# Kernel optimization log

Measured on AMD Instinct MI355X. Metric: run time of the kernel, lower is better.

The kernel has to match this reference:

```python
import jax, jax.numpy as jnp
import numpy as np

N, E = 100000, 800000
H, C = 4, 32
HC = H * C


def setup_inputs() -> dict:
    key = jax.random.key(0)
    ks = jax.random.split(key, 32)

    def lin(k, fi, fo):
        return jax.random.normal(k, (fi, fo), jnp.float32) / np.sqrt(fi)

    inp = {
        "x": jax.random.normal(ks[0], (N, 2), jnp.float32),
        "edge_index": jax.random.randint(ks[1], (2, E), 0, N, jnp.int64),
        "edge_attr": jax.random.normal(ks[2], (E, 1), jnp.float32),
        # layer 0 (in=2)
        "Wq0": lin(ks[3], 2, HC), "bq0": jnp.zeros((HC,), jnp.float32),
        "Wk0": lin(ks[4], 2, HC), "bk0": jnp.zeros((HC,), jnp.float32),
        "Wv0": lin(ks[5], 2, HC), "bv0": jnp.zeros((HC,), jnp.float32),
        "We0": lin(ks[6], 1, HC),
        "Ws0": lin(ks[7], 2, HC), "bs0": jnp.zeros((HC,), jnp.float32),
        # layer 1 (in=HC)
        "Wq1": lin(ks[8], HC, HC), "bq1": jnp.zeros((HC,), jnp.float32),
        "Wk1": lin(ks[9], HC, HC), "bk1": jnp.zeros((HC,), jnp.float32),
        "Wv1": lin(ks[10], HC, HC), "bv1": jnp.zeros((HC,), jnp.float32),
        "We1": lin(ks[11], 1, HC),
        "Ws1": lin(ks[12], HC, HC), "bs1": jnp.zeros((HC,), jnp.float32),
        # classifier
        "Wc1": lin(ks[13], HC, 128), "bc1": jnp.zeros((128,), jnp.float32),
        "Wc2": lin(ks[14], 128, 64), "bc2": jnp.zeros((64,), jnp.float32),
        "Wc3": lin(ks[15], 64, 1), "bc3": jnp.zeros((1,), jnp.float32),
    }
    return inp


def _tconv(x, src, dst, edge_attr, Wq, bq, Wk, bk, Wv, bv, We, Ws, bs):
    # PyG TransformerConv (concat=True, root_weight=True, beta=False)
    n = x.shape[0]
    q = (x @ Wq + bq).reshape(n, H, C)
    k = (x @ Wk + bk).reshape(n, H, C)
    v = (x @ Wv + bv).reshape(n, H, C)
    e = (edge_attr @ We).reshape(-1, H, C)            # [E,H,C]
    k_j = k[src] + e
    v_j = v[src] + e
    alpha = jnp.einsum("ehc,ehc->eh", q[dst], k_j) / np.sqrt(C)  # [E,H]
    m = jax.ops.segment_max(alpha, dst, num_segments=n)          # [n,H]
    m = jnp.where(jnp.isfinite(m), m, 0.0)            # nodes with no in-edges
    ex = jnp.exp(alpha - m[dst])
    denom = jax.ops.segment_sum(ex, dst, num_segments=n)
    w = ex / (denom[dst] + 1e-16)                      # per-edge softmax weight
    out = jax.ops.segment_sum(v_j * w[:, :, None], dst, num_segments=n)
    return out.reshape(n, HC) + x @ Ws + bs


def reference(x, edge_index, edge_attr,
              Wq0, bq0, Wk0, bk0, Wv0, bv0, We0, Ws0, bs0,
              Wq1, bq1, Wk1, bk1, Wv1, bv1, We1, Ws1, bs1,
              Wc1, bc1, Wc2, bc2, Wc3, bc3):
    src, dst = edge_index[0], edge_index[1]
    h = jax.nn.relu(_tconv(x, src, dst, edge_attr, Wq0, bq0, Wk0, bk0, Wv0, bv0, We0, Ws0, bs0))
    h = jax.nn.relu(_tconv(h, src, dst, edge_attr, Wq1, bq1, Wk1, bk1, Wv1, bv1, We1, Ws1, bs1))
    # classifier (dropout inactive in eval)
    h = jax.nn.relu(h @ Wc1 + bc1)
    h = jax.nn.relu(h @ Wc2 + bc2)
    return h @ Wc3 + bc3
```

## Files before the change

kernel.cpp:

```cpp
#include <hip/hip_runtime.h>
#include <hip/hip_bf16.h>
#include <cstdio>
#include <cstdint>


typedef short s16x8 __attribute__((ext_vector_type(8)));
typedef float f32x4 __attribute__((ext_vector_type(4)));

static inline int cdiv(int a, int b) { return (a + b - 1) / b; }

__device__ __forceinline__ float bflo(unsigned u) {
    union { unsigned i; float f; } x; x.i = u << 16; return x.f;
}
__device__ __forceinline__ float bfhi(unsigned u) {
    union { unsigned i; float f; } x; x.i = u & 0xffff0000u; return x.f;
}
__device__ __forceinline__ unsigned short f2b(float f) {
    __hip_bfloat16 h = __float2bfloat16(f);
    return *reinterpret_cast<unsigned short*>(&h);
}
__device__ __forceinline__ unsigned packbf(float lo, float hi) {
    return (unsigned)f2b(lo) | ((unsigned)f2b(hi) << 16);
}


__global__ __launch_bounds__(256) void hist_kernel(const int* __restrict__ dst, int E,
                                                   int* __restrict__ counts) {
    int e = blockIdx.x * 256 + threadIdx.x;
    if (e < E) atomicAdd(&counts[dst[e]], 1);
}

__global__ __launch_bounds__(256) void scan_sums(const int* __restrict__ counts, int n,
                                                 int* __restrict__ bsums) {
    __shared__ int red[256];
    int base = blockIdx.x * 2048 + threadIdx.x * 8;
    int s = 0;
#pragma unroll
    for (int j = 0; j < 8; ++j) {
        int i = base + j;
        if (i < n) s += counts[i];
    }
    red[threadIdx.x] = s;
    __syncthreads();
    for (int off = 128; off > 0; off >>= 1) {
        if (threadIdx.x < off) red[threadIdx.x] += red[threadIdx.x + off];
        __syncthreads();
    }
    if (threadIdx.x == 0) bsums[blockIdx.x] = red[0];
}

__global__ void scan_mid(int* bsums, int nb, int* offsets, int n) {
    if (blockIdx.x == 0 && threadIdx.x == 0) {
        int run = 0;
        for (int i = 0; i < nb; ++i) { int t = bsums[i]; bsums[i] = run; run += t; }
        offsets[n] = run;
    }
}

__global__ __launch_bounds__(256) void scan_out(const int* __restrict__ counts, int n,
                                                const int* __restrict__ bsums,
                                                int* __restrict__ offsets) {
    __shared__ int tsum[256];
    int base = blockIdx.x * 2048 + threadIdx.x * 8;
    int v[8];
    int s = 0;
#pragma unroll
    for (int j = 0; j < 8; ++j) {
        int i = base + j;
        v[j] = (i < n) ? counts[i] : 0;
        s += v[j];
    }
    tsum[threadIdx.x] = s;
    __syncthreads();
    for (int off = 1; off < 256; off <<= 1) {
        int x = (threadIdx.x >= (unsigned)off) ? tsum[threadIdx.x - off] : 0;
        __syncthreads();
        tsum[threadIdx.x] += x;
        __syncthreads();
    }
    int excl = tsum[threadIdx.x] - s + bsums[blockIdx.x];
#pragma unroll
    for (int j = 0; j < 8; ++j) {
        int i = base + j;
        if (i < n) { offsets[i] = excl; excl += v[j]; }
    }
}

__global__ __launch_bounds__(256) void scatter_kernel(const int* __restrict__ src,
                                                      const int* __restrict__ dst,
                                                      const float* __restrict__ ea, int E,
                                                      const int* __restrict__ offsets,
                                                      int* __restrict__ fill,
                                                      int* __restrict__ csr_src,
                                                      float* __restrict__ csr_ea) {
    int e = blockIdx.x * 256 + threadIdx.x;
    if (e >= E) return;
    int d = dst[e];
    int p = offsets[d] + atomicAdd(&fill[d], 1);
    csr_src[p] = src[e];
    csr_ea[p] = ea[e];
}


__global__ __launch_bounds__(256) void pack_w_kernel(
    const float* __restrict__ Wq1, const float* __restrict__ Wk1,
    const float* __restrict__ Wv1, const float* __restrict__ Ws1,
    const float* __restrict__ Wc1, const float* __restrict__ Wc2,
    unsigned short* __restrict__ wpk) {
    int idx = blockIdx.x * 256 + threadIdx.x;
    if (idx >= 90112) return;
    int local, COLS;
    const float* W;
    if (idx < 81920) {
        int m = idx >> 14;
        local = idx & 16383;
        COLS = 128;
        W = (m == 0) ? Wq1 : (m == 1) ? Wk1 : (m == 2) ? Wv1 : (m == 3) ? Ws1 : Wc1;
    } else {
        local = idx - 81920;
        COLS = 64;
        W = Wc2;
    }
    int CT = COLS >> 4;
    int j = local & 7, lane = (local >> 3) & 63, t = local >> 9;
    int ct = t % CT, kc = t / CT;
    int k = kc * 32 + ((lane >> 4) << 3) + j;
    int nn = (ct << 4) + (lane & 15);
    wpk[idx] = f2b(W[k * COLS + nn]);
}


__global__ void prep0_kernel(const float* __restrict__ Wq, const float* __restrict__ bq,
                             const float* __restrict__ Wk, const float* __restrict__ bk,
                             const float* __restrict__ We, float* __restrict__ gcoef) {
    int t = threadIdx.x;
    if (t >= 48) return;
    int h = t / 12, r = t % 12, i = r >> 2, j = r & 3;
    const float* A = (i == 0) ? Wq : (i == 1) ? (Wq + 128) : bq;
    const float* B = (j == 0) ? Wk : (j == 1) ? (Wk + 128) : (j == 2) ? We : bk;
    float s = 0.f;
    for (int c = 0; c < 32; ++c) s += A[h * 32 + c] * B[h * 32 + c];
    gcoef[h * 12 + i * 4 + j] = s * 0.17677669529663687f;
}


__global__ __launch_bounds__(256) void agg0_kernel(
    const float* __restrict__ x, const float* __restrict__ gcoef,
    float4* __restrict__ agg4,
    const int* __restrict__ offsets, const int* __restrict__ csr_src,
    const float* __restrict__ csr_ea, int n_nodes) {
    int tid = blockIdx.x * 256 + threadIdx.x;
    int n = tid >> 2, h = tid & 3;
    if (n >= n_nodes) return;
    float2 xn = ((const float2*)x)[n];
    const float4* G4 = (const float4*)gcoef;
    float4 g0 = G4[h * 3 + 0], g1 = G4[h * 3 + 1], g2 = G4[h * 3 + 2];
    float c0 = fmaf(xn.y, g1.x, fmaf(xn.x, g0.x, g2.x));
    float c1 = fmaf(xn.y, g1.y, fmaf(xn.x, g0.y, g2.y));
    float c2 = fmaf(xn.y, g1.z, fmaf(xn.x, g0.z, g2.z));
    float c3 = fmaf(xn.y, g1.w, fmaf(xn.x, g0.w, g2.w));
    int beg = offsets[n], end = offsets[n + 1];
    float m = -1e30f, d = 0.f, X0 = 0.f, X1 = 0.f, EA = 0.f;
    for (int j = beg; j < end; ++j) {
        int s = csr_src[j];
        float e = csr_ea[j];
        float2 xs = ((const float2*)x)[s];
        float al = fmaf(c0, xs.x, fmaf(c1, xs.y, fmaf(c2, e, c3)));
        float nm = fmaxf(m, al);
        float cc = __expf(m - nm), w = __expf(al - nm);
        d = fmaf(d, cc, w);
        X0 = fmaf(X0, cc, w * xs.x);
        X1 = fmaf(X1, cc, w * xs.y);
        EA = fmaf(EA, cc, w * e);
        m = nm;
    }
    agg4[(size_t)n * 4 + h] = make_float4(X0, X1, EA, d);
}


__global__ __launch_bounds__(256) void expand0_kernel(
    const float* __restrict__ x, const float4* __restrict__ agg4,
    const float* __restrict__ Wv, const float* __restrict__ bv,
    const float* __restrict__ We, const float* __restrict__ Ws,
    const float* __restrict__ bs, uint2* __restrict__ H0, int n_nodes) {
    int gid = blockIdx.x * 256 + threadIdx.x;
    int n = gid >> 5, g = gid & 31;
    if (n >= n_nodes) return;
    int h = g >> 3;
    float4 ag = agg4[(size_t)n * 4 + h];
    float inv = 1.f / (ag.w + 1e-16f);
    float2 xn = ((const float2*)x)[n];
    float4 wv0 = ((const float4*)Wv)[g], wv1 = ((const float4*)(Wv + 128))[g];
    float4 we = ((const float4*)We)[g], bv4 = ((const float4*)bv)[g];
    float4 ws0 = ((const float4*)Ws)[g], ws1 = ((const float4*)(Ws + 128))[g];
    float4 bs4 = ((const float4*)bs)[g];
    float o0 = fmaf(wv0.x, ag.x, fmaf(wv1.x, ag.y, fmaf(we.x, ag.z, bv4.x * ag.w))) * inv
             + fmaf(xn.x, ws0.x, fmaf(xn.y, ws1.x, bs4.x));
    float o1 = fmaf(wv0.y, ag.x, fmaf(wv1.y, ag.y, fmaf(we.y, ag.z, bv4.y * ag.w))) * inv
             + fmaf(xn.x, ws0.y, fmaf(xn.y, ws1.y, bs4.y));
    float o2 = fmaf(wv0.z, ag.x, fmaf(wv1.z, ag.y, fmaf(we.z, ag.z, bv4.z * ag.w))) * inv
             + fmaf(xn.x, ws0.z, fmaf(xn.y, ws1.z, bs4.z));
    float o3 = fmaf(wv0.w, ag.x, fmaf(wv1.w, ag.y, fmaf(we.w, ag.z, bv4.w * ag.w))) * inv
             + fmaf(xn.x, ws0.w, fmaf(xn.y, ws1.w, bs4.w));
    uint2 o;
    o.x = packbf(fmaxf(o0, 0.f), fmaxf(o1, 0.f));
    o.y = packbf(fmaxf(o2, 0.f), fmaxf(o3, 0.f));
    H0[(size_t)n * 32 + g] = o;
}


__global__ __launch_bounds__(256) void agg1_kernel(
    const uint2* __restrict__ Q2, const uint2* __restrict__ K2,
    const uint2* __restrict__ V2, const float* __restrict__ We,
    const uint2* __restrict__ S2, uint2* __restrict__ Hout,
    const int* __restrict__ offsets, const int* __restrict__ csr_src,
    const float* __restrict__ csr_ea, int n_nodes) {
    int wid = threadIdx.x >> 6, lane = threadIdx.x & 63;
    int h = lane & 31, half = lane >> 5;
    int n = blockIdx.x * 4 + wid;
    if (n >= n_nodes) return;
    size_t rb = (size_t)n * 32;
    const float rsc = 0.17677669529663687f;
    uint2 qp = Q2[rb + h];
    float q0 = bflo(qp.x) * rsc, q1 = bfhi(qp.x) * rsc;
    float q2 = bflo(qp.y) * rsc, q3 = bfhi(qp.y) * rsc;
    float4 we4 = ((const float4*)We)[h];
    float qwe = fmaf(q3, we4.w, fmaf(q2, we4.z, fmaf(q1, we4.y, q0 * we4.x)));
    qwe += __shfl_xor(qwe, 1);
    qwe += __shfl_xor(qwe, 2);
    qwe += __shfl_xor(qwe, 4);
    int beg = __builtin_amdgcn_readfirstlane(offsets[n]);
    int end = __builtin_amdgcn_readfirstlane(offsets[n + 1]);
    float mA = -1e30f, dA = 0.f, x0A = 0.f, x1A = 0.f, x2A = 0.f, x3A = 0.f, eAs = 0.f;
    float mB = -1e30f, dB = 0.f, x0B = 0.f, x1B = 0.f, x2B = 0.f, x3B = 0.f, eBs = 0.f;
    int nq = (end - beg + 3) >> 2;
    for (int it = 0; it < nq; ++it) {
        int jA = beg + 4 * it + half;
        int jB = jA + 2;
        bool vA = jA < end, vB = jB < end;
        int jmA = vA ? jA : beg, jmB = vB ? jB : beg;
        int sA = csr_src[jmA], sB = csr_src[jmB];
        float eaA = csr_ea[jmA], eaB = csr_ea[jmB];
        uint2 kA = K2[(size_t)sA * 32 + h], vA2 = V2[(size_t)sA * 32 + h];
        uint2 kB = K2[(size_t)sB * 32 + h], vB2 = V2[(size_t)sB * 32 + h];
        {
            float p = fmaf(q3, bfhi(kA.y), fmaf(q2, bflo(kA.y),
                      fmaf(q1, bfhi(kA.x), q0 * bflo(kA.x))));
            p += __shfl_xor(p, 1);
            p += __shfl_xor(p, 2);
            p += __shfl_xor(p, 4);
            float al = fmaf(eaA, qwe, p);
            al = vA ? al : -3.0e38f;
            float nm = fmaxf(mA, al);
            float cc = __expf(mA - nm), w = __expf(al - nm);
            dA = fmaf(dA, cc, w);
            x0A = fmaf(x0A, cc, w * bflo(vA2.x));
            x1A = fmaf(x1A, cc, w * bfhi(vA2.x));
            x2A = fmaf(x2A, cc, w * bflo(vA2.y));
            x3A = fmaf(x3A, cc, w * bfhi(vA2.y));
            eAs = fmaf(eAs, cc, w * eaA);
            mA = nm;
        }
        {
            float p = fmaf(q3, bfhi(kB.y), fmaf(q2, bflo(kB.y),
                      fmaf(q1, bfhi(kB.x), q0 * bflo(kB.x))));
            p += __shfl_xor(p, 1);
            p += __shfl_xor(p, 2);
            p += __shfl_xor(p, 4);
            float al = fmaf(eaB, qwe, p);
            al = vB ? al : -3.0e38f;
            float nm = fmaxf(mB, al);
            float cc = __expf(mB - nm), w = __expf(al - nm);
            dB = fmaf(dB, cc, w);
            x0B = fmaf(x0B, cc, w * bflo(vB2.x));
            x1B = fmaf(x1B, cc, w * bfhi(vB2.x));
            x2B = fmaf(x2B, cc, w * bflo(vB2.y));
            x3B = fmaf(x3B, cc, w * bfhi(vB2.y));
            eBs = fmaf(eBs, cc, w * eaB);
            mB = nm;
        }
    }
    float M = fmaxf(mA, mB);
    float cA = __expf(mA - M), cB = __expf(mB - M);
    float d = fmaf(dA, cA, dB * cB);
    float a0 = fmaf(x0A, cA, x0B * cB);
    float a1 = fmaf(x1A, cA, x1B * cB);
    float a2 = fmaf(x2A, cA, x2B * cB);
    float a3 = fmaf(x3A, cA, x3B * cB);
    float ea = fmaf(eAs, cA, eBs * cB);
    float mo = __shfl_xor(M, 32);
    float dd = __shfl_xor(d, 32);
    float b0 = __shfl_xor(a0, 32), b1 = __shfl_xor(a1, 32);
    float b2 = __shfl_xor(a2, 32), b3 = __shfl_xor(a3, 32);
    float eo = __shfl_xor(ea, 32);
    float MM = fmaxf(M, mo);
    float c0 = __expf(M - MM), c1 = __expf(mo - MM);
    d = d * c0 + dd * c1;
    a0 = a0 * c0 + b0 * c1; a1 = a1 * c0 + b1 * c1;
    a2 = a2 * c0 + b2 * c1; a3 = a3 * c0 + b3 * c1;
    ea = ea * c0 + eo * c1;
    float inv = 1.f / (d + 1e-16f);
    uint2 sp = S2[rb + h];
    if (half == 0) {
        uint2 o;
        o.x = packbf(fmaxf(fmaf((a0 + we4.x * ea), inv, bflo(sp.x)), 0.f),
                     fmaxf(fmaf((a1 + we4.y * ea), inv, bfhi(sp.x)), 0.f));
        o.y = packbf(fmaxf(fmaf((a2 + we4.z * ea), inv, bflo(sp.y)), 0.f),
                     fmaxf(fmaf((a3 + we4.w * ea), inv, bfhi(sp.y)), 0.f));
        Hout[rb + h] = o;
    }
}


__global__ __launch_bounds__(256) void gemm4_kernel(
    const unsigned short* __restrict__ Hb, int n_nodes,
    const unsigned short* __restrict__ wpk,
    const float* __restrict__ B0, unsigned short* __restrict__ O0,
    const float* __restrict__ B1, unsigned short* __restrict__ O1,
    const float* __restrict__ B2, unsigned short* __restrict__ O2,
    const float* __restrict__ B3, unsigned short* __restrict__ O3) {
    int wid = threadIdx.x >> 6, lane = threadIdx.x & 63;
    int lr = lane & 15, lk = lane >> 4;
    int rbase = blockIdx.x * 128 + wid * 32;
    s16x8 b[2][4];
#pragma unroll
    for (int nt = 0; nt < 2; ++nt) {
        int row = min(rbase + nt * 16 + lr, n_nodes - 1);
        const s16x8* hp = (const s16x8*)(Hb + (size_t)row * 128);
#pragma unroll
        for (int kc = 0; kc < 4; ++kc) b[nt][kc] = hp[kc * 4 + lk];
    }
    const float* Bm[4] = {B0, B1, B2, B3};
    unsigned short* Om[4] = {O0, O1, O2, O3};
#pragma unroll
    for (int mm = 0; mm < 4; ++mm) {
        const s16x8* wp = (const s16x8*)(wpk + mm * 16384);
        f32x4 acc[2][8];
#pragma unroll
        for (int nt = 0; nt < 2; ++nt)
#pragma unroll
            for (int ct = 0; ct < 8; ++ct) acc[nt][ct] = (f32x4){0.f, 0.f, 0.f, 0.f};
#pragma unroll
        for (int kc = 0; kc < 4; ++kc) {
#pragma unroll
            for (int ct = 0; ct < 8; ++ct) {
                s16x8 a = wp[(kc * 8 + ct) * 64 + lane];
                acc[0][ct] = __builtin_amdgcn_mfma_f32_16x16x32_bf16(a, b[0][kc], acc[0][ct], 0, 0, 0);
                acc[1][ct] = __builtin_amdgcn_mfma_f32_16x16x32_bf16(a, b[1][kc], acc[1][ct], 0, 0, 0);
            }
        }
        const float* Bp = Bm[mm];
        unsigned short* Op = Om[mm];
#pragma unroll
        for (int ct = 0; ct < 8; ++ct) {
            float4 bb = *(const float4*)(Bp + ct * 16 + lk * 4);
#pragma unroll
            for (int nt = 0; nt < 2; ++nt) {
                int node = rbase + nt * 16 + lr;
                if (node < n_nodes) {
                    uint2 o;
                    o.x = packbf(acc[nt][ct][0] + bb.x, acc[nt][ct][1] + bb.y);
                    o.y = packbf(acc[nt][ct][2] + bb.z, acc[nt][ct][3] + bb.w);
                    ((uint2*)(Op + (size_t)node * 128))[ct * 4 + lk] = o;
                }
            }
        }
    }
}


__global__ __launch_bounds__(256) void classifier_kernel(
    const unsigned short* __restrict__ H1b, int n_nodes,
    const unsigned short* __restrict__ wc1p, const float* __restrict__ bc1,
    const unsigned short* __restrict__ wc2p, const float* __restrict__ bc2,
    const float* __restrict__ Wc3, const float* __restrict__ bc3,
    float* __restrict__ out) {
    __shared__ char lds_raw[4 * 16 * 272];
    int wid = threadIdx.x >> 6, lane = threadIdx.x & 63;
    int lr = lane & 15, lk = lane >> 4;
    int nb = blockIdx.x * 64 + wid * 16;
    char* tile = lds_raw + wid * 16 * 272;

    s16x8 b[4];
    {
        int row = min(nb + lr, n_nodes - 1);
        const s16x8* hp = (const s16x8*)(H1b + (size_t)row * 128);
#pragma unroll
        for (int kc = 0; kc < 4; ++kc) b[kc] = hp[kc * 4 + lk];
    }
    f32x4 acc[8];
#pragma unroll
    for (int ct = 0; ct < 8; ++ct) acc[ct] = (f32x4){0.f, 0.f, 0.f, 0.f};
#pragma unroll
    for (int kc = 0; kc < 4; ++kc)
#pragma unroll
        for (int ct = 0; ct < 8; ++ct) {
            s16x8 a = ((const s16x8*)wc1p)[(kc * 8 + ct) * 64 + lane];
            acc[ct] = __builtin_amdgcn_mfma_f32_16x16x32_bf16(a, b[kc], acc[ct], 0, 0, 0);
        }
#pragma unroll
    for (int ct = 0; ct < 8; ++ct) {
        float4 bb = *(const float4*)(bc1 + ct * 16 + lk * 4);
        uint2 o;
        o.x = packbf(fmaxf(acc[ct][0] + bb.x, 0.f), fmaxf(acc[ct][1] + bb.y, 0.f));
        o.y = packbf(fmaxf(acc[ct][2] + bb.z, 0.f), fmaxf(acc[ct][3] + bb.w, 0.f));
        *(uint2*)(tile + lr * 272 + ct * 32 + lk * 8) = o;
    }
    __syncthreads();
    s16x8 b2[4];
#pragma unroll
    for (int kc = 0; kc < 4; ++kc)
        b2[kc] = *(const s16x8*)(tile + lr * 272 + kc * 64 + lk * 16);
    f32x4 acc2[4];
#pragma unroll
    for (int ct = 0; ct < 4; ++ct) acc2[ct] = (f32x4){0.f, 0.f, 0.f, 0.f};
#pragma unroll
    for (int kc = 0; kc < 4; ++kc)
#pragma unroll
        for (int ct = 0; ct < 4; ++ct) {
            s16x8 a = ((const s16x8*)wc2p)[(kc * 4 + ct) * 64 + lane];
            acc2[ct] = __builtin_amdgcn_mfma_f32_16x16x32_bf16(a, b2[kc], acc2[ct], 0, 0, 0);
        }
    float part = 0.f;
#pragma unroll
    for (int ct = 0; ct < 4; ++ct) {
        int ch0 = ct * 16 + lk * 4;
        float4 bb = *(const float4*)(bc2 + ch0);
        float4 w3 = *(const float4*)(Wc3 + ch0);
        part += fmaxf(acc2[ct][0] + bb.x, 0.f) * w3.x;
        part += fmaxf(acc2[ct][1] + bb.y, 0.f) * w3.y;
        part += fmaxf(acc2[ct][2] + bb.z, 0.f) * w3.z;
        part += fmaxf(acc2[ct][3] + bb.w, 0.f) * w3.w;
    }
    part += __shfl_xor(part, 16);
    part += __shfl_xor(part, 32);
    if (lk == 0) {
        int node = nb + lr;
        if (node < n_nodes) out[node] = part + bc3[0];
    }
}


extern "C" void kernel_launch(void* const* d_in, const int* in_sizes, int n_in,
                              void* d_out, int out_size, void* d_ws, size_t ws_size,
                              hipStream_t stream) {
    const float* x = (const float*)d_in[0];
    const int* ei = (const int*)d_in[1];
    const float* ea = (const float*)d_in[2];
    const float *Wq0 = (const float*)d_in[3], *bq0 = (const float*)d_in[4];
    const float *Wk0 = (const float*)d_in[5], *bk0 = (const float*)d_in[6];
    const float *Wv0 = (const float*)d_in[7], *bv0 = (const float*)d_in[8];
    const float* We0 = (const float*)d_in[9];
    const float *Ws0 = (const float*)d_in[10], *bs0 = (const float*)d_in[11];
    const float *Wq1 = (const float*)d_in[12], *bq1 = (const float*)d_in[13];
    const float *Wk1 = (const float*)d_in[14], *bk1 = (const float*)d_in[15];
    const float *Wv1 = (const float*)d_in[16], *bv1 = (const float*)d_in[17];
    const float* We1 = (const float*)d_in[18];
    const float *Ws1 = (const float*)d_in[19], *bs1 = (const float*)d_in[20];
    const float *Wc1 = (const float*)d_in[21], *bc1 = (const float*)d_in[22];
    const float *Wc2 = (const float*)d_in[23], *bc2 = (const float*)d_in[24];
    const float *Wc3 = (const float*)d_in[25], *bc3 = (const float*)d_in[26];

    const int N = in_sizes[0] / 2;
    const int E = in_sizes[2];
    const int* src = ei;
    const int* dst = ei + E;

    size_t NM = (size_t)N * 128;
    float4* agg4 = (float4*)d_ws;
    float* gcoef = (float*)(agg4 + (size_t)N * 4);
    unsigned short* H0b = (unsigned short*)(gcoef + 64);
    unsigned short* Qb = H0b + NM;
    unsigned short* Kb = Qb + NM;
    unsigned short* Vb = Kb + NM;
    unsigned short* S1b = Vb + NM;
    unsigned short* wpk = S1b + NM;
    int* counts = (int*)(wpk + 90112);
    int* fill = counts + N;
    int* offsets = fill + N;
    int* bsums = offsets + N + 1;
    int* csr_src = bsums + 256;
    float* csr_ea = (float*)(csr_src + E);
    size_t need = (size_t)((char*)(csr_ea + E) - (char*)d_ws);
    if (need > ws_size) {
        fprintf(stderr, "kernel_launch: ws too small (need %zu, have %zu)\n", need, ws_size);
        return;
    }

    const int NB_SCAN = cdiv(N, 2048);

    hipMemsetAsync(counts, 0, (size_t)N * 8, stream);
    hist_kernel<<<cdiv(E, 256), 256, 0, stream>>>(dst, E, counts);
    scan_sums<<<NB_SCAN, 256, 0, stream>>>(counts, N, bsums);
    scan_mid<<<1, 64, 0, stream>>>(bsums, NB_SCAN, offsets, N);
    scan_out<<<NB_SCAN, 256, 0, stream>>>(counts, N, bsums, offsets);
    scatter_kernel<<<cdiv(E, 256), 256, 0, stream>>>(src, dst, ea, E, offsets, fill,
                                                     csr_src, csr_ea);
    pack_w_kernel<<<cdiv(90112, 256), 256, 0, stream>>>(Wq1, Wk1, Wv1, Ws1, Wc1, Wc2, wpk);
    prep0_kernel<<<1, 64, 0, stream>>>(Wq0, bq0, Wk0, bk0, We0, gcoef);

    agg0_kernel<<<cdiv(N * 4, 256), 256, 0, stream>>>(
        x, gcoef, agg4, offsets, csr_src, csr_ea, N);
    expand0_kernel<<<cdiv(N * 32, 256), 256, 0, stream>>>(
        x, agg4, Wv0, bv0, We0, Ws0, bs0, (uint2*)H0b, N);

    gemm4_kernel<<<cdiv(N, 128), 256, 0, stream>>>(
        H0b, N, wpk, bq1, Qb, bk1, Kb, bv1, Vb, bs1, S1b);
    agg1_kernel<<<cdiv(N, 4), 256, 0, stream>>>(
        (const uint2*)Qb, (const uint2*)Kb, (const uint2*)Vb, We1,
        (const uint2*)S1b, (uint2*)S1b, offsets, csr_src, csr_ea, N);

    classifier_kernel<<<cdiv(N, 64), 256, 0, stream>>>(
        S1b, N, wpk + 65536, bc1, wpk + 81920, bc2, Wc3, bc3, (float*)d_out);
}
```

Before: 402.7 us.

## Drop online softmax max tracking, interleave K/V rows, fuse prep and scatter fill

Replaces the running-max online softmax in both aggregation kernels with plain exp2 accumulation, clamping logits to 72 and folding log2(e) into the scale. This removes the rescale exps and extra FMAs per edge. K and V are interleaved into one 256-wide row so each edge gathers both from one neighbourhood, and CSR stores precomputed byte offsets (src<<9). The scatter kernel reuses the counts array via atomicSub, which drops the fill buffer and halves the memset. prep0 is merged into pack_w as an extra block, and agg1 runs as one 64-thread block per node. Skipping the max subtraction risks overflow or precision loss if logits are large, which the clamp only partly guards against.

Result: faster. 385.3 us (-4.3%).

```diff
diff --git a/kernel.cpp b/kernel.cpp
--- a/kernel.cpp
+++ b/kernel.cpp
@@ -8,6 +8,10 @@
 typedef float f32x4 __attribute__((ext_vector_type(4)));
 
 static inline int cdiv(int a, int b) { return (a + b - 1) / b; }
+
+#define EXP2F(x) __builtin_amdgcn_exp2f(x)
+#define LOG2E 1.4426950408889634f
+#define RSC 0.17677669529663687f
 
 __device__ __forceinline__ float bflo(unsigned u) {
     union { unsigned i; float f; } x; x.i = u << 16; return x.f;
@@ -90,14 +94,15 @@
                                                       const int* __restrict__ dst,
                                                       const float* __restrict__ ea, int E,
                                                       const int* __restrict__ offsets,
-                                                      int* __restrict__ fill,
-                                                      int* __restrict__ csr_src,
+                                                      int* __restrict__ counts,
+                                                      int* __restrict__ csr_off,
                                                       float* __restrict__ csr_ea) {
     int e = blockIdx.x * 256 + threadIdx.x;
     if (e >= E) return;
     int d = dst[e];
-    int p = offsets[d] + atomicAdd(&fill[d], 1);
-    csr_src[p] = src[e];
+    int r = atomicSub(&counts[d], 1);
+    int p = offsets[d] + r - 1;
+    csr_off[p] = src[e] << 9;
     csr_ea[p] = ea[e];
 }
 
@@ -106,9 +111,23 @@
     const float* __restrict__ Wq1, const float* __restrict__ Wk1,
     const float* __restrict__ Wv1, const float* __restrict__ Ws1,
     const float* __restrict__ Wc1, const float* __restrict__ Wc2,
-    unsigned short* __restrict__ wpk) {
+    unsigned short* __restrict__ wpk,
+    const float* __restrict__ Wq0, const float* __restrict__ bq0,
+    const float* __restrict__ Wk0, const float* __restrict__ bk0,
+    const float* __restrict__ We0, float* __restrict__ gcoef) {
+    if (blockIdx.x == 352) {
+        int t = threadIdx.x;
+        if (t < 48) {
+            int h = t / 12, r = t % 12, i = r >> 2, j = r & 3;
+            const float* A = (i == 0) ? Wq0 : (i == 1) ? (Wq0 + 128) : bq0;
+            const float* B = (j == 0) ? Wk0 : (j == 1) ? (Wk0 + 128) : (j == 2) ? We0 : bk0;
+            float s = 0.f;
+            for (int c = 0; c < 32; ++c) s += A[h * 32 + c] * B[h * 32 + c];
+            gcoef[h * 12 + i * 4 + j] = s * (RSC * LOG2E);
+        }
+        return;
+    }
     int idx = blockIdx.x * 256 + threadIdx.x;
-    if (idx >= 90112) return;
     int local, COLS;
     const float* W;
     if (idx < 81920) {
@@ -130,24 +149,10 @@
 }
 
 
-__global__ void prep0_kernel(const float* __restrict__ Wq, const float* __restrict__ bq,
-                             const float* __restrict__ Wk, const float* __restrict__ bk,
-                             const float* __restrict__ We, float* __restrict__ gcoef) {
-    int t = threadIdx.x;
-    if (t >= 48) return;
-    int h = t / 12, r = t % 12, i = r >> 2, j = r & 3;
-    const float* A = (i == 0) ? Wq : (i == 1) ? (Wq + 128) : bq;
-    const float* B = (j == 0) ? Wk : (j == 1) ? (Wk + 128) : (j == 2) ? We : bk;
-    float s = 0.f;
-    for (int c = 0; c < 32; ++c) s += A[h * 32 + c] * B[h * 32 + c];
-    gcoef[h * 12 + i * 4 + j] = s * 0.17677669529663687f;
-}
-
-
 __global__ __launch_bounds__(256) void agg0_kernel(
     const float* __restrict__ x, const float* __restrict__ gcoef,
     float4* __restrict__ agg4,
-    const int* __restrict__ offsets, const int* __restrict__ csr_src,
+    const int* __restrict__ offsets, const int* __restrict__ csr_off,
     const float* __restrict__ csr_ea, int n_nodes) {
     int tid = blockIdx.x * 256 + threadIdx.x;
     int n = tid >> 2, h = tid & 3;
@@ -160,19 +165,17 @@
     float c2 = fmaf(xn.y, g1.z, fmaf(xn.x, g0.z, g2.z));
     float c3 = fmaf(xn.y, g1.w, fmaf(xn.x, g0.w, g2.w));
     int beg = offsets[n], end = offsets[n + 1];
-    float m = -1e30f, d = 0.f, X0 = 0.f, X1 = 0.f, EA = 0.f;
+    float d = 0.f, X0 = 0.f, X1 = 0.f, EA = 0.f;
     for (int j = beg; j < end; ++j) {
-        int s = csr_src[j];
+        int off = csr_off[j];
         float e = csr_ea[j];
-        float2 xs = ((const float2*)x)[s];
+        float2 xs = *(const float2*)((const char*)x + (off >> 6));
         float al = fmaf(c0, xs.x, fmaf(c1, xs.y, fmaf(c2, e, c3)));
-        float nm = fmaxf(m, al);
-        float cc = __expf(m - nm), w = __expf(al - nm);
-        d = fmaf(d, cc, w);
-        X0 = fmaf(X0, cc, w * xs.x);
-        X1 = fmaf(X1, cc, w * xs.y);
-        EA = fmaf(EA, cc, w * e);
-        m = nm;
+        float w = EXP2F(fminf(al, 72.f));
+        d += w;
+        X0 = fmaf(w, xs.x, X0);
+        X1 = fmaf(w, xs.y, X1);
+        EA = fmaf(w, e, EA);
     }
     agg4[(size_t)n * 4 + h] = make_float4(X0, X1, EA, d);
 }
@@ -209,21 +212,21 @@
 }
 
 
-__global__ __launch_bounds__(256) void agg1_kernel(
-    const uint2* __restrict__ Q2, const uint2* __restrict__ K2,
-    const uint2* __restrict__ V2, const float* __restrict__ We,
-    const uint2* __restrict__ S2, uint2* __restrict__ Hout,
-    const int* __restrict__ offsets, const int* __restrict__ csr_src,
-    const float* __restrict__ csr_ea, int n_nodes) {
-    int wid = threadIdx.x >> 6, lane = threadIdx.x & 63;
+__global__ __launch_bounds__(64) void agg1_kernel(
+    const uint2* __restrict__ Q2, const unsigned short* __restrict__ KV,
+    const float* __restrict__ We, const uint2* __restrict__ S2,
+    uint2* __restrict__ Hout, const int* __restrict__ offsets,
+    const int* __restrict__ csr_off, const float* __restrict__ csr_ea,
+    int n_nodes) {
+    int lane = threadIdx.x & 63;
     int h = lane & 31, half = lane >> 5;
-    int n = blockIdx.x * 4 + wid;
+    int n = blockIdx.x;
     if (n >= n_nodes) return;
     size_t rb = (size_t)n * 32;
-    const float rsc = 0.17677669529663687f;
+    const float sc = RSC * LOG2E;
     uint2 qp = Q2[rb + h];
-    float q0 = bflo(qp.x) * rsc, q1 = bfhi(qp.x) * rsc;
-    float q2 = bflo(qp.y) * rsc, q3 = bfhi(qp.y) * rsc;
+    float q0 = bflo(qp.x) * sc, q1 = bfhi(qp.x) * sc;
+    float q2 = bflo(qp.y) * sc, q3 = bfhi(qp.y) * sc;
     float4 we4 = ((const float4*)We)[h];
     float qwe = fmaf(q3, we4.w, fmaf(q2, we4.z, fmaf(q1, we4.y, q0 * we4.x)));
     qwe += __shfl_xor(qwe, 1);
@@ -231,35 +234,35 @@
     qwe += __shfl_xor(qwe, 4);
     int beg = __builtin_amdgcn_readfirstlane(offsets[n]);
     int end = __builtin_amdgcn_readfirstlane(offsets[n + 1]);
-    float mA = -1e30f, dA = 0.f, x0A = 0.f, x1A = 0.f, x2A = 0.f, x3A = 0.f, eAs = 0.f;
-    float mB = -1e30f, dB = 0.f, x0B = 0.f, x1B = 0.f, x2B = 0.f, x3B = 0.f, eBs = 0.f;
-    int nq = (end - beg + 3) >> 2;
-    for (int it = 0; it < nq; ++it) {
-        int jA = beg + 4 * it + half;
-        int jB = jA + 2;
-        bool vA = jA < end, vB = jB < end;
-        int jmA = vA ? jA : beg, jmB = vB ? jB : beg;
-        int sA = csr_src[jmA], sB = csr_src[jmB];
-        float eaA = csr_ea[jmA], eaB = csr_ea[jmB];
-        uint2 kA = K2[(size_t)sA * 32 + h], vA2 = V2[(size_t)sA * 32 + h];
-        uint2 kB = K2[(size_t)sB * 32 + h], vB2 = V2[(size_t)sB * 32 + h];
+    float dA = 0.f, a0A = 0.f, a1A = 0.f, a2A = 0.f, a3A = 0.f, eA = 0.f;
+    float dB = 0.f, a0B = 0.f, a1B = 0.f, a2B = 0.f, a3B = 0.f, eB = 0.f;
+    int lane_b = h << 3;
+    for (int j = beg + half; j < end; j += 4) {
+        int jB = j + 2;
+        bool vB = jB < end;
+        int jmB = vB ? jB : j;
+        int offA = csr_off[j], offB = csr_off[jmB];
+        float eaA = csr_ea[j], eaB = csr_ea[jmB];
+        const char* kvA = (const char*)KV + (size_t)(unsigned)offA + lane_b;
+        const char* kvB = (const char*)KV + (size_t)(unsigned)offB + lane_b;
+        uint2 kA = *(const uint2*)kvA;
+        uint2 vA = *(const uint2*)(kvA + 256);
+        uint2 kB = *(const uint2*)kvB;
+        uint2 vB2 = *(const uint2*)(kvB + 256);
         {
             float p = fmaf(q3, bfhi(kA.y), fmaf(q2, bflo(kA.y),
                       fmaf(q1, bfhi(kA.x), q0 * bflo(kA.x))));
             p += __shfl_xor(p, 1);
             p += __shfl_xor(p, 2);
             p += __shfl_xor(p, 4);
-            float al = fmaf(eaA, qwe, p);
-            al = vA ? al : -3.0e38f;
-            float nm = fmaxf(mA, al);
-            float cc = __expf(mA - nm), w = __expf(al - nm);
-            dA = fmaf(dA, cc, w);
-            x0A = fmaf(x0A, cc, w * bflo(vA2.x));
-            x1A = fmaf(x1A, cc, w * bfhi(vA2.x));
-            x2A = fmaf(x2A, cc, w * bflo(vA2.y));
-            x3A = fmaf(x3A, cc, w * bfhi(vA2.y));
-            eAs = fmaf(eAs, cc, w * eaA);
-            mA = nm;
+            float al = fminf(fmaf(eaA, qwe, p), 72.f);
+            float w = EXP2F(al);
+            dA += w;
+            a0A = fmaf(w, bflo(vA.x), a0A);
+            a1A = fmaf(w, bfhi(vA.x), a1A);
+            a2A = fmaf(w, bflo(vA.y), a2A);
+            a3A = fmaf(w, bfhi(vA.y), a3A);
+            eA = fmaf(w, eaA, eA);
         }
         {
             float p = fmaf(q3, bfhi(kB.y), fmaf(q2, bflo(kB.y),
@@ -269,44 +272,32 @@
             p += __shfl_xor(p, 4);
             float al = fmaf(eaB, qwe, p);
             al = vB ? al : -3.0e38f;
-            float nm = fmaxf(mB, al);
-            float cc = __expf(mB - nm), w = __expf(al - nm);
-            dB = fmaf(dB, cc, w);
-            x0B = fmaf(x0B, cc, w * bflo(vB2.x));
-            x1B = fmaf(x1B, cc, w * bfhi(vB2.x));
-            x2B = fmaf(x2B, cc, w * bflo(vB2.y));
-            x3B = fmaf(x3B, cc, w * bfhi(vB2.y));
-            eBs = fmaf(eBs, cc, w * eaB);
-            mB = nm;
-        }
-    }
-    float M = fmaxf(mA, mB);
-    float cA = __expf(mA - M), cB = __expf(mB - M);
-    float d = fmaf(dA, cA, dB * cB);
-    float a0 = fmaf(x0A, cA, x0B * cB);
-    float a1 = fmaf(x1A, cA, x1B * cB);
-    float a2 = fmaf(x2A, cA, x2B * cB);
-    float a3 = fmaf(x3A, cA, x3B * cB);
-    float ea = fmaf(eAs, cA, eBs * cB);
-    float mo = __shfl_xor(M, 32);
-    float dd = __shfl_xor(d, 32);
-    float b0 = __shfl_xor(a0, 32), b1 = __shfl_xor(a1, 32);
-    float b2 = __shfl_xor(a2, 32), b3 = __shfl_xor(a3, 32);
-    float eo = __shfl_xor(ea, 32);
-    float MM = fmaxf(M, mo);
-    float c0 = __expf(M - MM), c1 = __expf(mo - MM);
-    d = d * c0 + dd * c1;
-    a0 = a0 * c0 + b0 * c1; a1 = a1 * c0 + b1 * c1;
-    a2 = a2 * c0 + b2 * c1; a3 = a3 * c0 + b3 * c1;
-    ea = ea * c0 + eo * c1;
-    float inv = 1.f / (d + 1e-16f);
-    uint2 sp = S2[rb + h];
+            float w = EXP2F(fminf(al, 72.f));
+            dB += w;
+            a0B = fmaf(w, bflo(vB2.x), a0B);
+            a1B = fmaf(w, bfhi(vB2.x), a1B);
+            a2B = fmaf(w, bflo(vB2.y), a2B);
+            a3B = fmaf(w, bfhi(vB2.y), a3B);
+            eB = fmaf(w, eaB, eB);
+        }
+    }
+    float d = dA + dB;
+    float a0 = a0A + a0B, a1 = a1A + a1B, a2 = a2A + a2B, a3 = a3A + a3B;
+    float ea = eA + eB;
+    d += __shfl_xor(d, 32);
+    a0 += __shfl_xor(a0, 32);
+    a1 += __shfl_xor(a1, 32);
+    a2 += __shfl_xor(a2, 32);
+    a3 += __shfl_xor(a3, 32);
+    ea += __shfl_xor(ea, 32);
     if (half == 0) {
+        float inv = 1.f / (d + 1e-16f);
+        uint2 sp = S2[rb + h];
         uint2 o;
-        o.x = packbf(fmaxf(fmaf((a0 + we4.x * ea), inv, bflo(sp.x)), 0.f),
-                     fmaxf(fmaf((a1 + we4.y * ea), inv, bfhi(sp.x)), 0.f));
-        o.y = packbf(fmaxf(fmaf((a2 + we4.z * ea), inv, bflo(sp.y)), 0.f),
-                     fmaxf(fmaf((a3 + we4.w * ea), inv, bfhi(sp.y)), 0.f));
+        o.x = packbf(fmaxf(fmaf(a0 + we4.x * ea, inv, bflo(sp.x)), 0.f),
+                     fmaxf(fmaf(a1 + we4.y * ea, inv, bfhi(sp.x)), 0.f));
+        o.y = packbf(fmaxf(fmaf(a2 + we4.z * ea, inv, bflo(sp.y)), 0.f),
+                     fmaxf(fmaf(a3 + we4.w * ea, inv, bfhi(sp.y)), 0.f));
         Hout[rb + h] = o;
     }
 }
@@ -315,10 +306,10 @@
 __global__ __launch_bounds__(256) void gemm4_kernel(
     const unsigned short* __restrict__ Hb, int n_nodes,
     const unsigned short* __restrict__ wpk,
-    const float* __restrict__ B0, unsigned short* __restrict__ O0,
-    const float* __restrict__ B1, unsigned short* __restrict__ O1,
-    const float* __restrict__ B2, unsigned short* __restrict__ O2,
-    const float* __restrict__ B3, unsigned short* __restrict__ O3) {
+    const float* __restrict__ B0, unsigned short* __restrict__ O0, int ld0,
+    const float* __restrict__ B1, unsigned short* __restrict__ O1, int ld1,
+    const float* __restrict__ B2, unsigned short* __restrict__ O2, int ld2,
+    const float* __restrict__ B3, unsigned short* __restrict__ O3, int ld3) {
     int wid = threadIdx.x >> 6, lane = threadIdx.x & 63;
     int lr = lane & 15, lk = lane >> 4;
     int rbase = blockIdx.x * 128 + wid * 32;
@@ -332,6 +323,7 @@
     }
     const float* Bm[4] = {B0, B1, B2, B3};
     unsigned short* Om[4] = {O0, O1, O2, O3};
+    int ldm[4] = {ld0, ld1, ld2, ld3};
 #pragma unroll
     for (int mm = 0; mm < 4; ++mm) {
         const s16x8* wp = (const s16x8*)(wpk + mm * 16384);
@@ -351,6 +343,7 @@
         }
         const float* Bp = Bm[mm];
         unsigned short* Op = Om[mm];
+        int ld = ldm[mm];
 #pragma unroll
         for (int ct = 0; ct < 8; ++ct) {
             float4 bb = *(const float4*)(Bp + ct * 16 + lk * 4);
@@ -361,7 +354,7 @@
                     uint2 o;
                     o.x = packbf(acc[nt][ct][0] + bb.x, acc[nt][ct][1] + bb.y);
                     o.y = packbf(acc[nt][ct][2] + bb.z, acc[nt][ct][3] + bb.w);
-                    ((uint2*)(Op + (size_t)node * 128))[ct * 4 + lk] = o;
+                    ((uint2*)(Op + (size_t)node * ld))[ct * 4 + lk] = o;
                 }
             }
         }
@@ -471,16 +464,14 @@
     float* gcoef = (float*)(agg4 + (size_t)N * 4);
     unsigned short* H0b = (unsigned short*)(gcoef + 64);
     unsigned short* Qb = H0b + NM;
-    unsigned short* Kb = Qb + NM;
-    unsigned short* Vb = Kb + NM;
-    unsigned short* S1b = Vb + NM;
+    unsigned short* KV = Qb + NM;
+    unsigned short* S1b = KV + 2 * NM;
     unsigned short* wpk = S1b + NM;
     int* counts = (int*)(wpk + 90112);
-    int* fill = counts + N;
-    int* offsets = fill + N;
+    int* offsets = counts + N;
     int* bsums = offsets + N + 1;
-    int* csr_src = bsums + 256;
-    float* csr_ea = (float*)(csr_src + E);
+    int* csr_off = bsums + 256;
+    float* csr_ea = (float*)(csr_off + E);
     size_t need = (size_t)((char*)(csr_ea + E) - (char*)d_ws);
     if (need > ws_size) {
         fprintf(stderr, "kernel_launch: ws too small (need %zu, have %zu)\n", need, ws_size);
@@ -489,26 +480,30 @@
 
     const int NB_SCAN = cdiv(N, 2048);
 
-    hipMemsetAsync(counts, 0, (size_t)N * 8, stream);
+    hipMemsetAsync(counts, 0, (size_t)N * 4, stream);
     hist_kernel<<<cdiv(E, 256), 256, 0, stream>>>(dst, E, counts);
     scan_sums<<<NB_SCAN, 256, 0, stream>>>(counts, N, bsums);
     scan_mid<<<1, 64, 0, stream>>>(bsums, NB_SCAN, offsets, N);
     scan_out<<<NB_SCAN, 256, 0, stream>>>(counts, N, bsums, offsets);
-    scatter_kernel<<<cdiv(E, 256), 256, 0, stream>>>(src, dst, ea, E, offsets, fill,
-                                                     csr_src, csr_ea);
-    pack_w_kernel<<<cdiv(90112, 256), 256, 0, stream>>>(Wq1, Wk1, Wv1, Ws1, Wc1, Wc2, wpk);
-    prep0_kernel<<<1, 64, 0, stream>>>(Wq0, bq0, Wk0, bk0, We0, gcoef);
+    scatter_kernel<<<cdiv(E, 256), 256, 0, stream>>>(src, dst, ea, E, offsets, counts,
+                                                     csr_off, csr_ea);
+    pack_w_kernel<<<353, 256, 0, stream>>>(Wq1, Wk1, Wv1, Ws1, Wc1, Wc2, wpk,
+                                           Wq0, bq0, Wk0, bk0, We0, gcoef);
 
     agg0_kernel<<<cdiv(N * 4, 256), 256, 0, stream>>>(
-        x, gcoef, agg4, offsets, csr_src, csr_ea, N);
+        x, gcoef, agg4, offsets, csr_off, csr_ea, N);
     expand0_kernel<<<cdiv(N * 32, 256), 256, 0, stream>>>(
         x, agg4, Wv0, bv0, We0, Ws0, bs0, (uint2*)H0b, N);
 
     gemm4_kernel<<<cdiv(N, 128), 256, 0, stream>>>(
-        H0b, N, wpk, bq1, Qb, bk1, Kb, bv1, Vb, bs1, S1b);
-    agg1_kernel<<<cdiv(N, 4), 256, 0, stream>>>(
-        (const uint2*)Qb, (const uint2*)Kb, (const uint2*)Vb, We1,
-        (const uint2*)S1b, (uint2*)S1b, offsets, csr_src, csr_ea, N);
+        H0b, N, wpk,
+        bq1, Qb, 128,
+        bk1, KV, 256,
+        bv1, KV + 128, 256,
+        bs1, S1b, 128);
+    agg1_kernel<<<N, 64, 0, stream>>>(
+        (const uint2*)Qb, KV, We1, (const uint2*)S1b, (uint2*)S1b,
+        offsets, csr_off, csr_ea, N);
 
     classifier_kernel<<<cdiv(N, 64), 256, 0, stream>>>(
         S1b, N, wpk + 65536, bc1, wpk + 81920, bc2, Wc3, bc3, (float*)d_out);
```
